# Optimization experiments

Hardware: AMD Instinct MI355X
Metric: run time of the kernel (lower is better)

## Reference

```python
import jax, jax.numpy as jnp
import numpy as np

# Config (matches init_kwargs)
V = 32000      # vocab_size
H = 1024       # hidden_size
NH = 16        # num_heads
NKV = 4        # num_kv_heads
L = 4          # num_layers
FF = 4096      # intermediate_size
MAXPOS = 2048
HD = H // NH   # head_dim = 64
KVD = H * NKV // NH  # kv projection dim = 256
EPS = 1e-5


def setup_inputs() -> dict:
    key = jax.random.key(0)
    ks = iter(jax.random.split(key, 64))
    B, T = 1, 2048
    std = 0.02

    def w(shape):
        return jax.random.normal(next(ks), shape, dtype=jnp.float32) * std

    inp = {
        "input_ids": jax.random.randint(next(ks), (B, T), 0, V),
        "attention_mask": jnp.zeros((B, T), dtype=jnp.float32),
        "tok_emb": w((V, H)),
        "pos_emb": w((MAXPOS, H)),
        # stacked per-layer params; Linear weights stored as [in, out]
        "qW": w((L, H, H)),   "qb": jnp.zeros((L, H)),
        "kW": w((L, H, KVD)), "kb": jnp.zeros((L, KVD)),
        "vW": w((L, H, KVD)), "vb": jnp.zeros((L, KVD)),
        "oW": w((L, H, H)),   "ob": jnp.zeros((L, H)),
        "m1W": w((L, H, FF)), "m1b": jnp.zeros((L, FF)),
        "m2W": w((L, FF, H)), "m2b": jnp.zeros((L, H)),
        "ln1g": jnp.ones((L, H)), "ln1b": jnp.zeros((L, H)),
        "ln2g": jnp.ones((L, H)), "ln2b": jnp.zeros((L, H)),
        "lnfg": jnp.ones((H,)),   "lnfb": jnp.zeros((H,)),
        "headW": w((H, V)),  # head: Linear(H, V, bias=False), stored [in,out]
    }
    return inp


def _layer_norm(x, g, b):
    m = jnp.mean(x, axis=-1, keepdims=True)
    v = jnp.mean(jnp.square(x - m), axis=-1, keepdims=True)
    return (x - m) * jax.lax.rsqrt(v + EPS) * g + b


def _gqa_attn(x, mask, qW, qb, kW, kb, vW, vb, oW, ob):
    B, T, _ = x.shape
    G = NH // NKV  # query groups per kv head
    q = (x @ qW + qb).reshape(B, T, NH, HD).transpose(0, 2, 1, 3)        # [B,NH,T,HD]
    q = q.reshape(B, NKV, G, T, HD)                                      # [B,NKV,G,T,HD]
    k = (x @ kW + kb).reshape(B, T, NKV, HD).transpose(0, 2, 1, 3)       # [B,NKV,T,HD]
    v = (x @ vW + vb).reshape(B, T, NKV, HD).transpose(0, 2, 1, 3)       # [B,NKV,T,HD]
    # naive full score tensor [B,NKV,G,T,T] (as in the original module)
    scores = jnp.einsum("bkgqd,bksd->bkgqs", q, k) / jnp.sqrt(jnp.float32(HD))
    scores = scores + mask[:, None, None, None, :]  # additive mask over keys
    attn = jax.nn.softmax(scores, axis=-1)
    out = jnp.einsum("bkgqs,bksd->bkgqd", attn, v)                       # [B,NKV,G,T,HD]
    out = out.reshape(B, NH, T, HD).transpose(0, 2, 1, 3).reshape(B, T, H)
    return out @ oW + ob


def reference(input_ids, attention_mask, tok_emb, pos_emb,
              qW, qb, kW, kb, vW, vb, oW, ob,
              m1W, m1b, m2W, m2b,
              ln1g, ln1b, ln2g, ln2b, lnfg, lnfb, headW):
    B, T = input_ids.shape
    x = tok_emb[input_ids] + pos_emb[jnp.arange(T)][None, :, :]  # [B,T,H]
    for i in range(L):
        h = _layer_norm(x, ln1g[i], ln1b[i])
        x = x + _gqa_attn(h, attention_mask, qW[i], qb[i], kW[i], kb[i],
                          vW[i], vb[i], oW[i], ob[i])
        h = _layer_norm(x, ln2g[i], ln2b[i])
        h = jax.nn.gelu(h @ m1W[i] + m1b[i], approximate=False) @ m2W[i] + m2b[i]
        x = x + h
    x = _layer_norm(x, lnfg, lnfb)
    logits = x @ headW  # [B,T,V]
    return logits
```

## Files before the change

### kernel.cpp

```cpp
#include <hip/hip_runtime.h>
#include <stdint.h>
#include <math.h>

typedef __attribute__((ext_vector_type(8))) short bf16x8;
typedef __attribute__((ext_vector_type(4))) short bf16x4;
typedef __attribute__((ext_vector_type(4))) float f32x4;

__device__ __forceinline__ short f2bf(float f) {
  unsigned u = __builtin_bit_cast(unsigned, f);
  unsigned r = u + 0x7fffu + ((u >> 16) & 1u);
  return (short)(r >> 16);
}

__device__ __forceinline__ f32x4 mfma16(bf16x8 a, bf16x8 b, f32x4 c) {
  return __builtin_amdgcn_mfma_f32_16x16x32_bf16(a, b, c, 0, 0, 0);
}

__device__ __forceinline__ void gload16(const void* g, void* l) {
  __builtin_amdgcn_global_load_lds((const __attribute__((address_space(1))) void*)g,
                                   (__attribute__((address_space(3))) void*)l, 16, 0, 0);
}

__device__ __forceinline__ int swz(int row, int col) {
  return row * 64 + (((col >> 3) ^ (row & 7)) << 3) + (col & 7);
}

__global__ __launch_bounds__(256) void embed_k(const int* __restrict__ ids,
                                               const float* __restrict__ tok,
                                               const float* __restrict__ pos,
                                               float* __restrict__ x) {
  const int t = threadIdx.x, w = t >> 6, lane = t & 63;
  const int row = blockIdx.x * 4 + w;
  const int id = ids[row];
#pragma unroll
  for (int i = 0; i < 4; ++i) {
    const int c = (i * 64 + lane) * 4;
    const float4 a = *reinterpret_cast<const float4*>(tok + (size_t)id * 1024 + c);
    const float4 b = *reinterpret_cast<const float4*>(pos + (size_t)row * 1024 + c);
    float4 o = make_float4(a.x + b.x, a.y + b.y, a.z + b.z, a.w + b.w);
    *reinterpret_cast<float4*>(x + (size_t)row * 1024 + c) = o;
  }
}

__global__ __launch_bounds__(256) void ln_k(const float* __restrict__ x,
                                            const float* __restrict__ gw,
                                            const float* __restrict__ bw,
                                            short* __restrict__ out) {
  const int t = threadIdx.x, w = t >> 6, lane = t & 63;
  const int row = blockIdx.x * 4 + w;
  float4 v[4];
  float s = 0.f, q = 0.f;
#pragma unroll
  for (int i = 0; i < 4; ++i) {
    v[i] = *reinterpret_cast<const float4*>(x + (size_t)row * 1024 + (i * 64 + lane) * 4);
    s += v[i].x + v[i].y + v[i].z + v[i].w;
    q += v[i].x * v[i].x + v[i].y * v[i].y + v[i].z * v[i].z + v[i].w * v[i].w;
  }
#pragma unroll
  for (int o = 32; o > 0; o >>= 1) { s += __shfl_xor(s, o); q += __shfl_xor(q, o); }
  const float mean = s * (1.f / 1024.f);
  const float var  = q * (1.f / 1024.f) - mean * mean;
  const float rstd = rsqrtf(var + 1e-5f);
#pragma unroll
  for (int i = 0; i < 4; ++i) {
    const int c = (i * 64 + lane) * 4;
    const float4 gv = *reinterpret_cast<const float4*>(gw + c);
    const float4 bv = *reinterpret_cast<const float4*>(bw + c);
    bf16x4 ov = { f2bf((v[i].x - mean) * rstd * gv.x + bv.x),
                  f2bf((v[i].y - mean) * rstd * gv.y + bv.y),
                  f2bf((v[i].z - mean) * rstd * gv.z + bv.z),
                  f2bf((v[i].w - mean) * rstd * gv.w + bv.w) };
    *reinterpret_cast<bf16x4*>(out + (size_t)row * 1024 + c) = ov;
  }
}

__global__ __launch_bounds__(256) void tcvt_k(const float* __restrict__ W,
                                              short* __restrict__ Wt,
                                              int N, size_t inStride, size_t outStride,
                                              int rowOff, int ldOut, float scale) {
  __shared__ float T[128][68];
  const float* Win = W + blockIdx.z * inStride;
  short* Wout = Wt + blockIdx.z * outStride;
  const int n0 = blockIdx.x * 64, k0 = blockIdx.y * 128;
  const int t = threadIdx.x;
  const int nc = (t & 15) * 4, kr = t >> 4;
#pragma unroll
  for (int p = 0; p < 8; ++p) {
    const float4 v = *reinterpret_cast<const float4*>(Win + (size_t)(k0 + kr + 16 * p) * N + n0 + nc);
    T[kr + 16 * p][nc + 0] = v.x;
    T[kr + 16 * p][nc + 1] = v.y;
    T[kr + 16 * p][nc + 2] = v.z;
    T[kr + 16 * p][nc + 3] = v.w;
  }
  __syncthreads();
  const int n = t >> 2, ks = (t & 3) * 32;
  short tmp[32];
#pragma unroll
  for (int i = 0; i < 32; ++i) tmp[i] = f2bf(T[ks + i][n] * scale);
  short* op = Wout + (size_t)(rowOff + n0 + n) * ldOut + k0 + ks;
#pragma unroll
  for (int c = 0; c < 4; ++c)
    *reinterpret_cast<bf16x8*>(op + c * 8) = *reinterpret_cast<bf16x8*>(tmp + c * 8);
}

__global__ __launch_bounds__(256) void bqkv_k(const float* __restrict__ qb,
                                              const float* __restrict__ kb,
                                              const float* __restrict__ vb,
                                              float* __restrict__ o) {
  int l = blockIdx.y;
  int c = blockIdx.x * 256 + threadIdx.x;
  float v;
  if (c < 1024) v = qb[l * 1024 + c] * 0.125f;
  else if (c < 1280) v = kb[l * 256 + c - 1024];
  else v = vb[l * 256 + c - 1280];
  o[l * 1536 + c] = v;
}

__global__ __launch_bounds__(256) void vtr_k(const short* __restrict__ v, int vld,
                                             short* __restrict__ vt) {
  __shared__ short T[64][80];
  const int kvh = blockIdx.y;
  const int s0 = blockIdx.x * 64;
  const int t = threadIdx.x;
  const int row = t >> 3, ch = t & 7;
#pragma unroll
  for (int p = 0; p < 2; ++p) {
    int s = row + 32 * p;
    bf16x8 vv = *reinterpret_cast<const bf16x8*>(v + (size_t)(s0 + s) * vld + kvh * 64 + ch * 8);
    *reinterpret_cast<bf16x8*>(&T[s][ch * 8]) = vv;
  }
  __syncthreads();
#pragma unroll
  for (int p = 0; p < 2; ++p) {
    int d = row + 32 * p;
    short tmp[8];
#pragma unroll
    for (int i = 0; i < 8; ++i) tmp[i] = T[ch * 8 + i][d];
    *reinterpret_cast<bf16x8*>(vt + (size_t)(kvh * 64 + d) * 2048 + s0 + ch * 8) =
        *reinterpret_cast<bf16x8*>(tmp);
  }
}

template <int EPI, int XSWZ, int TILE>
__global__ __launch_bounds__(256, 4)
void gemm_bt(const short* __restrict__ A, const short* __restrict__ Wt,
             const float* __restrict__ bias, const float* __restrict__ resid,
             void* __restrict__ out, int M, int N, int K, int nbOff,
             short* __restrict__ vt) {
  constexpr int BN   = (TILE == 0) ? 128 : 64;
  constexpr int WN   = (TILE == 0) ? 64 : 32;
  constexpr int NT   = (TILE == 0) ? 4 : 2;
  constexpr int BISS = (TILE == 0) ? 4 : 2;
  __shared__ short As[128 * 64];
  __shared__ short Bs[BN * 64];
  const int t = threadIdx.x;
  const int lane = t & 63, w = t >> 6;
  const int g = lane >> 4, r = lane & 15;
  const int wr = w >> 1, wc = w & 1;

  int bx = blockIdx.x, by = blockIdx.y;
  if (XSWZ == 1) {
    const int nbx = gridDim.x, nby = gridDim.y, nwg = nbx * nby;
    const int bid = by * nbx + bx;
    const int q = nwg >> 3, rr = nwg & 7;
    const int xcd = bid & 7, loc = bid >> 3;
    const int sw = (xcd < rr ? xcd * (q + 1) : rr * (q + 1) + (xcd - rr) * q) + loc;
    by = sw % nby; bx = sw / nby;
  }
  const int m0 = by * 128, n0 = (bx + nbOff) * BN;

  f32x4 acc[4][NT];
#pragma unroll
  for (int i = 0; i < 4; ++i)
#pragma unroll
    for (int j = 0; j < NT; ++j) { f32x4 z = {0.f, 0.f, 0.f, 0.f}; acc[i][j] = z; }

  const int srow = lane >> 3, sslot = lane & 7;

  for (int k0 = 0; k0 < K; k0 += 64) {
#pragma unroll
    for (int i = 0; i < 4; ++i) {
      const int rowA = w * 32 + i * 8 + srow;
      const int colA = (sslot ^ (srow & 7)) << 3;
      gload16(A + (size_t)(m0 + rowA) * K + k0 + colA, &As[(w * 32 + i * 8) * 64]);
    }
#pragma unroll
    for (int i = 0; i < BISS; ++i) {
      const int rowB = w * (8 * BISS) + i * 8 + srow;
      const int colB = (sslot ^ (srow & 7)) << 3;
      gload16(Wt + (size_t)(n0 + rowB) * K + k0 + colB, &Bs[(w * (8 * BISS) + i * 8) * 64]);
    }
    __syncthreads();
#pragma unroll
    for (int kk = 0; kk < 64; kk += 32) {
      bf16x8 af[4], bfg[NT];
#pragma unroll
      for (int mt = 0; mt < 4; ++mt)
        af[mt] = *reinterpret_cast<const bf16x8*>(&As[swz(wr * 64 + mt * 16 + r, kk + g * 8)]);
#pragma unroll
      for (int nt = 0; nt < NT; ++nt)
        bfg[nt] = *reinterpret_cast<const bf16x8*>(&Bs[swz(wc * WN + nt * 16 + r, kk + g * 8)]);
#pragma unroll
      for (int mt = 0; mt < 4; ++mt)
#pragma unroll
        for (int nt = 0; nt < NT; ++nt)
          acc[mt][nt] = mfma16(af[mt], bfg[nt], acc[mt][nt]);
    }
    __syncthreads();
  }
#pragma unroll
  for (int nt = 0; nt < NT; ++nt) {
    const int col = n0 + wc * WN + nt * 16 + r;
    const float bv = (EPI == 3) ? 0.f : bias[col];
#pragma unroll
    for (int mt = 0; mt < 4; ++mt) {
      const int rowb = m0 + wr * 64 + mt * 16 + 4 * g;
      short vs[4];
#pragma unroll
      for (int j = 0; j < 4; ++j) {
        const int row = rowb + j;
        const size_t oi = (size_t)row * N + col;
        float vv = acc[mt][nt][j] + bv;
        if (EPI == 0) {
          ((short*)out)[oi] = f2bf(vv);
        } else if (EPI == 1) {
          vv = 0.5f * vv * (1.f + erff(vv * 0.70710678118654752f));
          ((short*)out)[oi] = f2bf(vv);
        } else if (EPI == 2) {
          ((float*)out)[oi] = resid[oi] + vv;
        } else if (EPI == 3) {
          ((float*)out)[oi] = vv;
        } else {
          short bb = f2bf(vv);
          ((short*)out)[oi] = bb;
          vs[j] = bb;
        }
      }
      if (EPI == 4 && col >= 1280) {
        bf16x4 pk = { vs[0], vs[1], vs[2], vs[3] };
        *reinterpret_cast<bf16x4*>(vt + (size_t)(col - 1280) * 2048 + rowb) = pk;
      }
    }
  }
}

template <int EPI>
__global__ __launch_bounds__(256)
void gemm_k(const short* __restrict__ A, const float* __restrict__ W,
            const float* __restrict__ bias, const float* resid, void* out,
            int M, int N, int K, float scale) {
  __shared__ short As[128 * 64];
  __shared__ short Bs[128 * 64];
  const int t = threadIdx.x;
  const int lane = t & 63;
  const int g = lane >> 4, r = lane & 15;
  const int wid = t >> 6, wr = wid >> 1, wc = wid & 1;
  const int m0 = blockIdx.y * 128, n0 = blockIdx.x * 128;
  f32x4 acc[4][4];
#pragma unroll
  for (int i = 0; i < 4; ++i)
#pragma unroll
    for (int j = 0; j < 4; ++j) { f32x4 z = {0.f, 0.f, 0.f, 0.f}; acc[i][j] = z; }
  const int arow = t >> 3, ac = t & 7;
  const int bnn = t >> 1, bkh = t & 1;
  for (int k0 = 0; k0 < K; k0 += 64) {
#pragma unroll
    for (int p = 0; p < 4; ++p) {
      int row = arow + 32 * p;
      bf16x8 av = *reinterpret_cast<const bf16x8*>(A + (size_t)(m0 + row) * K + k0 + ac * 8);
      *reinterpret_cast<bf16x8*>(&As[swz(row, ac * 8)]) = av;
    }
#pragma unroll
    for (int p = 0; p < 8; ++p) {
      int kg = 4 * (bkh + 2 * p);
      const float* wp = W + (size_t)(k0 + kg) * N + n0 + bnn;
      bf16x4 wv = { f2bf(wp[0]), f2bf(wp[(size_t)N]), f2bf(wp[(size_t)2 * N]), f2bf(wp[(size_t)3 * N]) };
      *reinterpret_cast<bf16x4*>(&Bs[swz(bnn, kg)]) = wv;
    }
    __syncthreads();
#pragma unroll
    for (int kk = 0; kk < 64; kk += 32) {
      bf16x8 af[4], bfg[4];
#pragma unroll
      for (int mt = 0; mt < 4; ++mt)
        af[mt] = *reinterpret_cast<const bf16x8*>(&As[swz(wr * 64 + mt * 16 + r, kk + g * 8)]);
#pragma unroll
      for (int nt = 0; nt < 4; ++nt)
        bfg[nt] = *reinterpret_cast<const bf16x8*>(&Bs[swz(wc * 64 + nt * 16 + r, kk + g * 8)]);
#pragma unroll
      for (int mt = 0; mt < 4; ++mt)
#pragma unroll
        for (int nt = 0; nt < 4; ++nt)
          acc[mt][nt] = mfma16(af[mt], bfg[nt], acc[mt][nt]);
    }
    __syncthreads();
  }
#pragma unroll
  for (int nt = 0; nt < 4; ++nt) {
    const int col = n0 + wc * 64 + nt * 16 + r;
    const float bv = (EPI == 3) ? 0.f : bias[col];
#pragma unroll
    for (int mt = 0; mt < 4; ++mt) {
#pragma unroll
      for (int j = 0; j < 4; ++j) {
        const int row = m0 + wr * 64 + mt * 16 + 4 * g + j;
        const size_t oi = (size_t)row * N + col;
        float vv = acc[mt][nt][j] + bv;
        if (EPI == 0) {
          ((short*)out)[oi] = f2bf(vv * scale);
        } else if (EPI == 1) {
          vv = 0.5f * vv * (1.f + erff(vv * 0.70710678118654752f));
          ((short*)out)[oi] = f2bf(vv);
        } else if (EPI == 2) {
          ((float*)out)[oi] = resid[oi] + vv;
        } else {
          ((float*)out)[oi] = vv;
        }
      }
    }
  }
}

__global__ __launch_bounds__(256) void attn_k(const short* __restrict__ q, int qld,
                                              const short* __restrict__ k, int kld,
                                              const short* __restrict__ vt,
                                              const float* __restrict__ mask,
                                              short* __restrict__ o) {
  __shared__ short Ks[2][64 * 64];
  __shared__ short Vs[2][64 * 64];
  const int t = threadIdx.x, lane = t & 63, w = t >> 6;
  const int g = lane >> 4, r = lane & 15;
  const int h = blockIdx.y, qb = blockIdx.x, kvh = h >> 2;
  const int qrow = qb * 64 + w * 16 + r;

  const short* qp = q + (size_t)qrow * qld + h * 64;
  bf16x8 qf0 = *reinterpret_cast<const bf16x8*>(qp + g * 8);
  bf16x8 qf1 = *reinterpret_cast<const bf16x8*>(qp + 32 + g * 8);

  const short* kbase = k + kvh * 64;
  const short* vbase = vt + (size_t)kvh * 64 * 2048;

  f32x4 oacc[4];
#pragma unroll
  for (int i = 0; i < 4; ++i) { f32x4 z = {0.f, 0.f, 0.f, 0.f}; oacc[i] = z; }
  float m_run = -INFINITY, l_run = 0.f;

  const int srow = w * 8 + (lane >> 3), schunk = lane & 7;

#pragma unroll
  for (int p = 0; p < 2; ++p) {
    const int rr = srow + 32 * p;
    const int cc = (schunk ^ (rr & 7)) << 3;
    gload16(kbase + (size_t)rr * kld + cc, (char*)Ks + p * 4096 + w * 1024);
    gload16(vbase + (size_t)rr * 2048 + cc, (char*)Vs + p * 4096 + w * 1024);
  }
  asm volatile("s_waitcnt vmcnt(0)" ::: "memory");
  __syncthreads();

  for (int it = 0; it < 32; ++it) {
    const int cur = it & 1;
    if (it < 31) {
      const int s1 = (it + 1) * 64;
#pragma unroll
      for (int p = 0; p < 2; ++p) {
        const int rr = srow + 32 * p;
        const int cc = (schunk ^ (rr & 7)) << 3;
        gload16(kbase + (size_t)(s1 + rr) * kld + cc,
                (char*)Ks + (cur ^ 1) * 8192 + p * 4096 + w * 1024);
        gload16(vbase + (size_t)rr * 2048 + s1 + cc,
                (char*)Vs + (cur ^ 1) * 8192 + p * 4096 + w * 1024);
      }
    }
    const int s0 = it * 64;
    const short* Kc = Ks[cur];
    const short* Vc = Vs[cur];

    f32x4 sa[4];
#pragma unroll
    for (int st = 0; st < 4; ++st) {
      bf16x8 kf0 = *reinterpret_cast<const bf16x8*>(&Kc[swz(st * 16 + r, g * 8)]);
      bf16x8 kf1 = *reinterpret_cast<const bf16x8*>(&Kc[swz(st * 16 + r, 32 + g * 8)]);
      f32x4 z = {0.f, 0.f, 0.f, 0.f};
      z = mfma16(kf0, qf0, z);
      z = mfma16(kf1, qf1, z);
      sa[st] = z;
    }
    float sv[16];
    float pmax = -INFINITY;
#pragma unroll
    for (int st = 0; st < 4; ++st) {
      const float4 mv = *reinterpret_cast<const float4*>(mask + s0 + st * 16 + 4 * g);
#pragma unroll
      for (int j = 0; j < 4; ++j) {
        float xx = sa[st][j] + ((const float*)&mv)[j];
        sv[st * 4 + j] = xx;
        pmax = fmaxf(pmax, xx);
      }
    }
    pmax = fmaxf(pmax, __shfl_xor(pmax, 16));
    pmax = fmaxf(pmax, __shfl_xor(pmax, 32));
    float m_new = fmaxf(m_run, pmax);
    float corr = __expf(m_run - m_new);
    float psum = 0.f;
    short pb[16];
#pragma unroll
    for (int i = 0; i < 16; ++i) {
      float p = __expf(sv[i] - m_new);
      psum += p;
      pb[i] = f2bf(p);
    }
    psum += __shfl_xor(psum, 16);
    psum += __shfl_xor(psum, 32);
    l_run = l_run * corr + psum;
    m_run = m_new;
#pragma unroll
    for (int dt = 0; dt < 4; ++dt)
#pragma unroll
      for (int j = 0; j < 4; ++j) oacc[dt][j] *= corr;

#pragma unroll
    for (int hs = 0; hs < 2; ++hs) {
      bf16x8 pf = { pb[hs * 8 + 0], pb[hs * 8 + 1], pb[hs * 8 + 2], pb[hs * 8 + 3],
                    pb[hs * 8 + 4], pb[hs * 8 + 5], pb[hs * 8 + 6], pb[hs * 8 + 7] };
#pragma unroll
      for (int dt = 0; dt < 4; ++dt) {
        int d = dt * 16 + r;
        int c1 = 4 * g + 32 * hs;
        bf16x4 va  = *reinterpret_cast<const bf16x4*>(&Vc[swz(d, c1)]);
        bf16x4 vb2 = *reinterpret_cast<const bf16x4*>(&Vc[swz(d, c1 + 16)]);
        bf16x8 vf = { va[0], va[1], va[2], va[3], vb2[0], vb2[1], vb2[2], vb2[3] };
        oacc[dt] = mfma16(vf, pf, oacc[dt]);
      }
    }
    asm volatile("s_waitcnt vmcnt(0)" ::: "memory");
    __syncthreads();
  }
  float inv = 1.f / l_run;
#pragma unroll
  for (int dt = 0; dt < 4; ++dt) {
    bf16x4 ov = { f2bf(oacc[dt][0] * inv), f2bf(oacc[dt][1] * inv),
                  f2bf(oacc[dt][2] * inv), f2bf(oacc[dt][3] * inv) };
    *reinterpret_cast<bf16x4*>(o + (size_t)qrow * 1024 + h * 64 + dt * 16 + 4 * g) = ov;
  }
}

extern "C" void kernel_launch(void* const* d_in, const int* in_sizes, int n_in,
                              void* d_out, int out_size, void* d_ws, size_t ws_size,
                              hipStream_t stream) {
  const int*   ids   = (const int*)d_in[0];
  const float* mask  = (const float*)d_in[1];
  const float* tok   = (const float*)d_in[2];
  const float* pos   = (const float*)d_in[3];
  const float* qW    = (const float*)d_in[4];
  const float* qbias = (const float*)d_in[5];
  const float* kW    = (const float*)d_in[6];
  const float* kbias = (const float*)d_in[7];
  const float* vW    = (const float*)d_in[8];
  const float* vbias = (const float*)d_in[9];
  const float* oW    = (const float*)d_in[10];
  const float* obias = (const float*)d_in[11];
  const float* m1W   = (const float*)d_in[12];
  const float* m1b   = (const float*)d_in[13];
  const float* m2W   = (const float*)d_in[14];
  const float* m2b   = (const float*)d_in[15];
  const float* ln1g  = (const float*)d_in[16];
  const float* ln1b  = (const float*)d_in[17];
  const float* ln2g  = (const float*)d_in[18];
  const float* ln2b  = (const float*)d_in[19];
  const float* lnfg  = (const float*)d_in[20];
  const float* lnfb  = (const float*)d_in[21];
  const float* headW = (const float*)d_in[22];
  float* out = (float*)d_out;

  char* ws = (char*)d_ws;
  float* x   = (float*)ws;
  short* xb  = (short*)(ws + 8388608ull);

  const size_t OFF_QKV  = 12582912ull;
  const size_t OFF_AO   = 18874368ull;
  const size_t OFF_FF   = 23068672ull;
  const size_t OFF_BQ   = 39845888ull;
  const size_t OFF_WQKV = 39870464ull;
  const size_t OFF_WO   = 52453376ull;
  const size_t OFF_WM1  = 60841984ull;
  const size_t OFF_WM2  = 94396416ull;
  const size_t OFF_WH   = 127950848ull;
  const size_t NEED     = 193486848ull;

  if (ws_size >= NEED) {
    short* qkv  = (short*)(ws + OFF_QKV);
    short* ao   = (short*)(ws + OFF_AO);
    short* ff   = (short*)(ws + OFF_FF);
    short* vt   = ff;
    float* bqv  = (float*)(ws + OFF_BQ);
    short* Wqkv = (short*)(ws + OFF_WQKV);
    short* Wo   = (short*)(ws + OFF_WO);
    short* Wm1  = (short*)(ws + OFF_WM1);
    short* Wm2  = (short*)(ws + OFF_WM2);
    short* Wh   = (short*)(ws + OFF_WH);

    tcvt_k<<<dim3(16, 8, 4), 256, 0, stream>>>(qW, Wqkv, 1024, 1048576ull, 1572864ull, 0, 1024, 0.125f);
    tcvt_k<<<dim3(4, 8, 4),  256, 0, stream>>>(kW, Wqkv, 256,  262144ull,  1572864ull, 1024, 1024, 1.f);
    tcvt_k<<<dim3(4, 8, 4),  256, 0, stream>>>(vW, Wqkv, 256,  262144ull,  1572864ull, 1280, 1024, 1.f);
    tcvt_k<<<dim3(16, 8, 4), 256, 0, stream>>>(oW, Wo, 1024, 1048576ull, 1048576ull, 0, 1024, 1.f);
    tcvt_k<<<dim3(64, 8, 4), 256, 0, stream>>>(m1W, Wm1, 4096, 4194304ull, 4194304ull, 0, 1024, 1.f);
    tcvt_k<<<dim3(16, 32, 4), 256, 0, stream>>>(m2W, Wm2, 1024, 4194304ull, 4194304ull, 0, 4096, 1.f);
    tcvt_k<<<dim3(500, 8, 1), 256, 0, stream>>>(headW, Wh, 32000, 0ull, 0ull, 0, 1024, 1.f);
    bqkv_k<<<dim3(6, 4), 256, 0, stream>>>(qbias, kbias, vbias, bqv);

    embed_k<<<512, 256, 0, stream>>>(ids, tok, pos, x);

    for (int l = 0; l < 4; ++l) {
      short* Wq_l  = Wqkv + (size_t)l * 1536 * 1024;
      short* Wo_l  = Wo   + (size_t)l * 1024 * 1024;
      short* Wm1_l = Wm1  + (size_t)l * 4096 * 1024;
      short* Wm2_l = Wm2  + (size_t)l * 1024 * 4096;

      ln_k<<<512, 256, 0, stream>>>(x, ln1g + l * 1024, ln1b + l * 1024, xb);
      gemm_bt<4, 0, 1><<<dim3(24, 16), 256, 0, stream>>>(xb, Wq_l, bqv + l * 1536, nullptr,
                                                         qkv, 2048, 1536, 1024, 0, vt);
      attn_k<<<dim3(32, 16), 256, 0, stream>>>(qkv, 1536, qkv + 1024, 1536, vt, mask, ao);
      gemm_bt<2, 0, 1><<<dim3(16, 16), 256, 0, stream>>>(ao, Wo_l, obias + l * 1024, x,
                                                         x, 2048, 1024, 1024, 0, nullptr);
      ln_k<<<512, 256, 0, stream>>>(x, ln2g + l * 1024, ln2b + l * 1024, xb);
      gemm_bt<1, 1, 1><<<dim3(64, 16), 256, 0, stream>>>(xb, Wm1_l, m1b + l * 4096, nullptr,
                                                         ff, 2048, 4096, 1024, 0, nullptr);
      gemm_bt<2, 1, 1><<<dim3(16, 16), 256, 0, stream>>>(ff, Wm2_l, m2b + l * 1024, x,
                                                         x, 2048, 1024, 4096, 0, nullptr);
    }
    ln_k<<<512, 256, 0, stream>>>(x, lnfg, lnfb, xb);
    gemm_bt<3, 1, 0><<<dim3(250, 16), 256, 0, stream>>>(xb, Wh, nullptr, nullptr,
                                                        out, 2048, 32000, 1024, 0, nullptr);
  } else {
    short* qbf = (short*)(ws + (12u << 20));
    short* kbf = (short*)(ws + (16u << 20));
    short* vbf = (short*)(ws + (17u << 20));
    short* ao  = (short*)(ws + (18u << 20));
    short* ff  = (short*)(ws + (22u << 20));
    short* vtf = (short*)(ws + (38u << 20));

    embed_k<<<512, 256, 0, stream>>>(ids, tok, pos, x);
    for (int l = 0; l < 4; ++l) {
      ln_k<<<512, 256, 0, stream>>>(x, ln1g + l * 1024, ln1b + l * 1024, xb);
      gemm_k<0><<<dim3(8, 16), 256, 0, stream>>>(xb, qW + (size_t)l * 1024 * 1024,
          qbias + l * 1024, nullptr, qbf, 2048, 1024, 1024, 0.125f);
      gemm_k<0><<<dim3(2, 16), 256, 0, stream>>>(xb, kW + (size_t)l * 1024 * 256,
          kbias + l * 256, nullptr, kbf, 2048, 256, 1024, 1.f);
      gemm_k<0><<<dim3(2, 16), 256, 0, stream>>>(xb, vW + (size_t)l * 1024 * 256,
          vbias + l * 256, nullptr, vbf, 2048, 256, 1024, 1.f);
      vtr_k<<<dim3(32, 4), 256, 0, stream>>>(vbf, 256, vtf);
      attn_k<<<dim3(32, 16), 256, 0, stream>>>(qbf, 1024, kbf, 256, vtf, mask, ao);
      gemm_k<2><<<dim3(8, 16), 256, 0, stream>>>(ao, oW + (size_t)l * 1024 * 1024,
          obias + l * 1024, x, x, 2048, 1024, 1024, 1.f);
      ln_k<<<512, 256, 0, stream>>>(x, ln2g + l * 1024, ln2b + l * 1024, xb);
      gemm_k<1><<<dim3(32, 16), 256, 0, stream>>>(xb, m1W + (size_t)l * 1024 * 4096,
          m1b + l * 4096, nullptr, ff, 2048, 4096, 1024, 1.f);
      gemm_k<2><<<dim3(8, 16), 256, 0, stream>>>(ff, m2W + (size_t)l * 4096 * 1024,
          m2b + l * 1024, x, x, 2048, 1024, 4096, 1.f);
    }
    ln_k<<<512, 256, 0, stream>>>(x, lnfg, lnfb, xb);
    gemm_k<3><<<dim3(250, 16), 256, 0, stream>>>(xb, headW, nullptr, nullptr, out,
        2048, 32000, 1024, 1.f);
  }
}
```

Baseline: 1.166 ms.

## Split-K the MLP down-projection and merge weight conversion kernels into one launch

The FF2 GEMM (K=4096) now runs as a split-K over two z-slices, each writing fp32 partials to a temporary buffer. A new combine kernel then adds the partials, bias and residual into x. This targets the low occupancy of the 256-block FF2 launch, at the cost of extra fp32 traffic and one more launch per layer. Separately, the seven weight transpose/convert launches are folded into a single table-driven launch to cut launch overhead and tail effects.

```diff
diff --git a/kernel.cpp b/kernel.cpp
--- a/kernel.cpp
+++ b/kernel.cpp
@@ -74,19 +74,34 @@
   }
 }
 
-__global__ __launch_bounds__(256) void tcvt_k(const float* __restrict__ W,
-                                              short* __restrict__ Wt,
-                                              int N, size_t inStride, size_t outStride,
-                                              int rowOff, int ldOut, float scale) {
+struct TSeg {
+  const float* src; short* dst;
+  unsigned long long inStride, outStride;
+  int N, nbx, nbxy, rowOff, ldOut, blkEnd;
+  float scale;
+};
+struct TTab { TSeg s[7]; };
+
+__global__ __launch_bounds__(256) void tcvt_all(TTab tab) {
+  const int b = blockIdx.x;
+  int si = 0;
+  while (b >= tab.s[si].blkEnd) ++si;
+  const TSeg sg = tab.s[si];
+  const int base = (si == 0) ? 0 : tab.s[si - 1].blkEnd;
+  int lb = b - base;
+  const int z = lb / sg.nbxy; lb -= z * sg.nbxy;
+  const int by = lb / sg.nbx;
+  const int bx = lb - by * sg.nbx;
+
   __shared__ float T[128][68];
-  const float* Win = W + blockIdx.z * inStride;
-  short* Wout = Wt + blockIdx.z * outStride;
-  const int n0 = blockIdx.x * 64, k0 = blockIdx.y * 128;
+  const float* Win = sg.src + (size_t)z * sg.inStride;
+  short* Wout = sg.dst + (size_t)z * sg.outStride;
+  const int n0 = bx * 64, k0 = by * 128;
   const int t = threadIdx.x;
   const int nc = (t & 15) * 4, kr = t >> 4;
 #pragma unroll
   for (int p = 0; p < 8; ++p) {
-    const float4 v = *reinterpret_cast<const float4*>(Win + (size_t)(k0 + kr + 16 * p) * N + n0 + nc);
+    const float4 v = *reinterpret_cast<const float4*>(Win + (size_t)(k0 + kr + 16 * p) * sg.N + n0 + nc);
     T[kr + 16 * p][nc + 0] = v.x;
     T[kr + 16 * p][nc + 1] = v.y;
     T[kr + 16 * p][nc + 2] = v.z;
@@ -96,8 +111,8 @@
   const int n = t >> 2, ks = (t & 3) * 32;
   short tmp[32];
 #pragma unroll
-  for (int i = 0; i < 32; ++i) tmp[i] = f2bf(T[ks + i][n] * scale);
-  short* op = Wout + (size_t)(rowOff + n0 + n) * ldOut + k0 + ks;
+  for (int i = 0; i < 32; ++i) tmp[i] = f2bf(T[ks + i][n] * sg.scale);
+  short* op = Wout + (size_t)(sg.rowOff + n0 + n) * sg.ldOut + k0 + ks;
 #pragma unroll
   for (int c = 0; c < 4; ++c)
     *reinterpret_cast<bf16x8*>(op + c * 8) = *reinterpret_cast<bf16x8*>(tmp + c * 8);
@@ -116,6 +131,26 @@
   o[l * 1536 + c] = v;
 }
 
+__global__ __launch_bounds__(256) void comb_k(const float* __restrict__ t0,
+                                              const float* __restrict__ t1,
+                                              const float* __restrict__ bias,
+                                              float* __restrict__ x) {
+  const int t = threadIdx.x, w = t >> 6, lane = t & 63;
+  const int row = blockIdx.x * 4 + w;
+#pragma unroll
+  for (int i = 0; i < 4; ++i) {
+    const int c = (i * 64 + lane) * 4;
+    const size_t o = (size_t)row * 1024 + c;
+    const float4 a = *reinterpret_cast<const float4*>(t0 + o);
+    const float4 b = *reinterpret_cast<const float4*>(t1 + o);
+    const float4 bb = *reinterpret_cast<const float4*>(bias + c);
+    const float4 xx = *reinterpret_cast<const float4*>(x + o);
+    float4 r = make_float4(xx.x + a.x + b.x + bb.x, xx.y + a.y + b.y + bb.y,
+                           xx.z + a.z + b.z + bb.z, xx.w + a.w + b.w + bb.w);
+    *reinterpret_cast<float4*>(x + o) = r;
+  }
+}
+
 __global__ __launch_bounds__(256) void vtr_k(const short* __restrict__ v, int vld,
                                              short* __restrict__ vt) {
   __shared__ short T[64][80];
@@ -145,8 +180,8 @@
 __global__ __launch_bounds__(256, 4)
 void gemm_bt(const short* __restrict__ A, const short* __restrict__ Wt,
              const float* __restrict__ bias, const float* __restrict__ resid,
-             void* __restrict__ out, int M, int N, int K, int nbOff,
-             short* __restrict__ vt) {
+             void* __restrict__ out, int M, int N, int K, int kBeg, int kEnd,
+             int nbOff, short* __restrict__ vt) {
   constexpr int BN   = (TILE == 0) ? 128 : 64;
   constexpr int WN   = (TILE == 0) ? 64 : 32;
   constexpr int NT   = (TILE == 0) ? 4 : 2;
@@ -168,6 +203,8 @@
     by = sw % nby; bx = sw / nby;
   }
   const int m0 = by * 128, n0 = (bx + nbOff) * BN;
+  const int kShift = (int)blockIdx.z * (kEnd - kBeg);
+  const size_t zOfs = (size_t)blockIdx.z * (size_t)M * (size_t)N;
 
   f32x4 acc[4][NT];
 #pragma unroll
@@ -177,7 +214,7 @@
 
   const int srow = lane >> 3, sslot = lane & 7;
 
-  for (int k0 = 0; k0 < K; k0 += 64) {
+  for (int k0 = kBeg + kShift; k0 < kEnd + kShift; k0 += 64) {
 #pragma unroll
     for (int i = 0; i < 4; ++i) {
       const int rowA = w * 32 + i * 8 + srow;
@@ -229,7 +266,7 @@
         } else if (EPI == 2) {
           ((float*)out)[oi] = resid[oi] + vv;
         } else if (EPI == 3) {
-          ((float*)out)[oi] = vv;
+          ((float*)out)[oi + zOfs] = vv;
         } else {
           short bb = f2bf(vv);
           ((short*)out)[oi] = bb;
@@ -485,7 +522,8 @@
   const size_t OFF_WM1  = 60841984ull;
   const size_t OFF_WM2  = 94396416ull;
   const size_t OFF_WH   = 127950848ull;
-  const size_t NEED     = 193486848ull;
+  const size_t OFF_TMP  = 193486848ull;
+  const size_t NEED     = 210264064ull;
 
   if (ws_size >= NEED) {
     short* qkv  = (short*)(ws + OFF_QKV);
@@ -498,14 +536,29 @@
     short* Wm1  = (short*)(ws + OFF_WM1);
     short* Wm2  = (short*)(ws + OFF_WM2);
     short* Wh   = (short*)(ws + OFF_WH);
-
-    tcvt_k<<<dim3(16, 8, 4), 256, 0, stream>>>(qW, Wqkv, 1024, 1048576ull, 1572864ull, 0, 1024, 0.125f);
-    tcvt_k<<<dim3(4, 8, 4),  256, 0, stream>>>(kW, Wqkv, 256,  262144ull,  1572864ull, 1024, 1024, 1.f);
-    tcvt_k<<<dim3(4, 8, 4),  256, 0, stream>>>(vW, Wqkv, 256,  262144ull,  1572864ull, 1280, 1024, 1.f);
-    tcvt_k<<<dim3(16, 8, 4), 256, 0, stream>>>(oW, Wo, 1024, 1048576ull, 1048576ull, 0, 1024, 1.f);
-    tcvt_k<<<dim3(64, 8, 4), 256, 0, stream>>>(m1W, Wm1, 4096, 4194304ull, 4194304ull, 0, 1024, 1.f);
-    tcvt_k<<<dim3(16, 32, 4), 256, 0, stream>>>(m2W, Wm2, 1024, 4194304ull, 4194304ull, 0, 4096, 1.f);
-    tcvt_k<<<dim3(500, 8, 1), 256, 0, stream>>>(headW, Wh, 32000, 0ull, 0ull, 0, 1024, 1.f);
+    float* tmp0 = (float*)(ws + OFF_TMP);
+    float* tmp1 = tmp0 + 2097152;
+
+    TTab tab;
+    int acc = 0;
+    auto seg = [&](int i, const float* src, short* dst, size_t inS, size_t outS,
+                   int N, int nbx, int nby, int nbz, int rowOff, int ldOut, float scale) {
+      acc += nbx * nby * nbz;
+      tab.s[i].src = src;      tab.s[i].dst = dst;
+      tab.s[i].inStride = inS; tab.s[i].outStride = outS;
+      tab.s[i].N = N;          tab.s[i].nbx = nbx;
+      tab.s[i].nbxy = nbx * nby;
+      tab.s[i].rowOff = rowOff; tab.s[i].ldOut = ldOut;
+      tab.s[i].blkEnd = acc;   tab.s[i].scale = scale;
+    };
+    seg(0, headW, Wh,   0ull,        0ull,        32000, 500, 8, 1, 0,    1024, 1.f);
+    seg(1, m1W,   Wm1,  4194304ull,  4194304ull,  4096,  64,  8, 4, 0,    1024, 1.f);
+    seg(2, m2W,   Wm2,  4194304ull,  4194304ull,  1024,  16, 32, 4, 0,    4096, 1.f);
+    seg(3, qW,    Wqkv, 1048576ull,  1572864ull,  1024,  16,  8, 4, 0,    1024, 0.125f);
+    seg(4, oW,    Wo,   1048576ull,  1048576ull,  1024,  16,  8, 4, 0,    1024, 1.f);
+    seg(5, kW,    Wqkv, 262144ull,   1572864ull,  256,   4,   8, 4, 1024, 1024, 1.f);
+    seg(6, vW,    Wqkv, 262144ull,   1572864ull,  256,   4,   8, 4, 1280, 1024, 1.f);
+    tcvt_all<<<acc, 256, 0, stream>>>(tab);
     bqkv_k<<<dim3(6, 4), 256, 0, stream>>>(qbias, kbias, vbias, bqv);
 
     embed_k<<<512, 256, 0, stream>>>(ids, tok, pos, x);
@@ -518,19 +571,20 @@
 
       ln_k<<<512, 256, 0, stream>>>(x, ln1g + l * 1024, ln1b + l * 1024, xb);
       gemm_bt<4, 0, 1><<<dim3(24, 16), 256, 0, stream>>>(xb, Wq_l, bqv + l * 1536, nullptr,
-                                                         qkv, 2048, 1536, 1024, 0, vt);
+                                                         qkv, 2048, 1536, 1024, 0, 1024, 0, vt);
       attn_k<<<dim3(32, 16), 256, 0, stream>>>(qkv, 1536, qkv + 1024, 1536, vt, mask, ao);
       gemm_bt<2, 0, 1><<<dim3(16, 16), 256, 0, stream>>>(ao, Wo_l, obias + l * 1024, x,
-                                                         x, 2048, 1024, 1024, 0, nullptr);
+                                                         x, 2048, 1024, 1024, 0, 1024, 0, nullptr);
       ln_k<<<512, 256, 0, stream>>>(x, ln2g + l * 1024, ln2b + l * 1024, xb);
       gemm_bt<1, 1, 1><<<dim3(64, 16), 256, 0, stream>>>(xb, Wm1_l, m1b + l * 4096, nullptr,
-                                                         ff, 2048, 4096, 1024, 0, nullptr);
-      gemm_bt<2, 1, 1><<<dim3(16, 16), 256, 0, stream>>>(ff, Wm2_l, m2b + l * 1024, x,
-                                                         x, 2048, 1024, 4096, 0, nullptr);
+                                                         ff, 2048, 4096, 1024, 0, 1024, 0, nullptr);
+      gemm_bt<3, 1, 1><<<dim3(16, 16, 2), 256, 0, stream>>>(ff, Wm2_l, nullptr, nullptr,
+                                                            tmp0, 2048, 1024, 4096, 0, 2048, 0, nullptr);
+      comb_k<<<512, 256, 0, stream>>>(tmp0, tmp1, m2b + l * 1024, x);
     }
     ln_k<<<512, 256, 0, stream>>>(x, lnfg, lnfb, xb);
     gemm_bt<3, 1, 0><<<dim3(250, 16), 256, 0, stream>>>(xb, Wh, nullptr, nullptr,
-                                                        out, 2048, 32000, 1024, 0, nullptr);
+                                                        out, 2048, 32000, 1024, 0, 1024, 0, nullptr);
   } else {
     short* qbf = (short*)(ws + (12u << 20));
     short* kbf = (short*)(ws + (16u << 20));
```

Result: faster. 988.2 us (-15.3%).
